# Optimization experiments

Hardware: AMD Instinct MI355X
Metric: run time of the kernel (lower is better)

The kernel has to match this reference:

```python
import jax, jax.numpy as jnp
import numpy as np

D_MODEL = 1024
NUM_HEADS = 16
D_K = D_MODEL // NUM_HEADS
B, S = 2, 2048
NEG = -1e9


def setup_inputs() -> dict:
    key = jax.random.key(0)
    ks = jax.random.split(key, 12)
    scale = 1.0 / np.sqrt(D_MODEL)
    inp = {
        'q': jax.random.normal(ks[0], (B, S, D_MODEL), jnp.float32),
        'k': jax.random.normal(ks[1], (B, S, D_MODEL), jnp.float32),
        'v': jax.random.normal(ks[2], (B, S, D_MODEL), jnp.float32),
        'mask': jax.random.randint(ks[3], (1, 1, S, S), 0, 2, jnp.int32),
        'wq_w': jax.random.normal(ks[4], (D_MODEL, D_MODEL), jnp.float32) * scale,
        'wq_b': jnp.zeros((D_MODEL,), jnp.float32),
        'wk_w': jax.random.normal(ks[5], (D_MODEL, D_MODEL), jnp.float32) * scale,
        'wk_b': jnp.zeros((D_MODEL,), jnp.float32),
        'wv_w': jax.random.normal(ks[6], (D_MODEL, D_MODEL), jnp.float32) * scale,
        'wv_b': jnp.zeros((D_MODEL,), jnp.float32),
        'wo_w': jax.random.normal(ks[7], (D_MODEL, D_MODEL), jnp.float32) * scale,
        'wo_b': jnp.zeros((D_MODEL,), jnp.float32),
    }
    return inp


def _split_heads(x):
    # [B,S,D] -> [B,H,S,d_k]
    b, s, _ = x.shape
    return x.reshape(b, s, NUM_HEADS, D_K).transpose(0, 2, 1, 3)


def reference(q, k, v, mask, wq_w, wq_b, wk_w, wk_b, wv_w, wv_b, wo_w, wo_b):
    # torch Linear: y = x @ W.T + b
    qh = _split_heads(q @ wq_w.T + wq_b)
    kh = _split_heads(k @ wk_w.T + wk_b)
    vh = _split_heads(v @ wv_w.T + wv_b)
    scores = jnp.einsum('bhqd,bhkd->bhqk', qh, kh) / jnp.sqrt(jnp.float32(D_K))
    scores = jnp.where(mask == 0, jnp.float32(NEG), scores)
    attn = jax.nn.softmax(scores, axis=-1)  # dropout p=0 (eval): no-op
    x = jnp.einsum('bhqk,bhkd->bhqd', attn, vh)
    x = x.transpose(0, 2, 1, 3).reshape(q.shape[0], q.shape[1], D_MODEL)
    return x @ wo_w.T + wo_b
```

## Files before the change

### kernel.cpp

```cpp
#include <hip/hip_runtime.h>
#include <hip/hip_bf16.h>
#include <stdint.h>

#define S_LEN  2048
#define DMODEL 1024
#define NHEADS 16
#define DKH    64
#define KDIM   1024

typedef __bf16 bf16x8 __attribute__((ext_vector_type(8)));
typedef float  floatx4 __attribute__((ext_vector_type(4)));
typedef unsigned short ushort8v __attribute__((ext_vector_type(8)));

__device__ inline void gll16(const __bf16* g, const __bf16* l) {
    __builtin_amdgcn_global_load_lds(
        (const __attribute__((address_space(1))) void*)g,
        (__attribute__((address_space(3))) void*)l, 16, 0, 0);
}

__device__ inline float fast_exp2(float x) {
#if __has_builtin(__builtin_amdgcn_exp2f)
    return __builtin_amdgcn_exp2f(x);
#else
    return exp2f(x);
#endif
}

__global__ __launch_bounds__(256) void convert_all_kernel(
    const float* __restrict__ q, const float* __restrict__ k, const float* __restrict__ v,
    const float* __restrict__ wq, const float* __restrict__ wk, const float* __restrict__ wv,
    const float* __restrict__ wo, __bf16* __restrict__ out) {
    const size_t i8 = ((size_t)blockIdx.x * 256 + threadIdx.x) * 8;
    const float* src;
    if (i8 < 4194304u)        src = q  + i8;
    else if (i8 < 8388608u)   src = k  + (i8 - 4194304u);
    else if (i8 < 12582912u)  src = v  + (i8 - 8388608u);
    else if (i8 < 13631488u)  src = wq + (i8 - 12582912u);
    else if (i8 < 14680064u)  src = wk + (i8 - 13631488u);
    else if (i8 < 15728640u)  src = wv + (i8 - 14680064u);
    else                      src = wo + (i8 - 15728640u);
    floatx4 a = *(const floatx4*)src;
    floatx4 b = *(const floatx4*)(src + 4);
    bf16x8 r;
#pragma unroll
    for (int i = 0; i < 4; ++i) { r[i] = (__bf16)a[i]; r[i + 4] = (__bf16)b[i]; }
    *(bf16x8*)(out + i8) = r;
}

__global__ __launch_bounds__(256) void maskpack_kernel(const int* __restrict__ M,
                                                       uint64_t* __restrict__ P) {
    const size_t i = (size_t)blockIdx.x * 256 + threadIdx.x;
    uint64_t bits = __ballot(M[i] != 0);
    if ((threadIdx.x & 63) == 0) P[i >> 6] = bits;
}

__global__ __launch_bounds__(256) void qkv_gemm(
    const __bf16* __restrict__ qb, const __bf16* __restrict__ kb, const __bf16* __restrict__ vb,
    const __bf16* __restrict__ wqw, const __bf16* __restrict__ wkw, const __bf16* __restrict__ wvw,
    const float* __restrict__ biasq, const float* __restrict__ biask, const float* __restrict__ biasv,
    __bf16* __restrict__ qh, __bf16* __restrict__ kh, __bf16* __restrict__ vt) {
    __shared__ __align__(16) __bf16 As[2 * 128 * 32];
    __shared__ __align__(16) __bf16 Bs[2 * 128 * 32];

    const int lane = threadIdx.x & 63;
    const int wave = threadIdx.x >> 6;
    const int quad = lane >> 4;
    const int l15  = lane & 15;

    const int bid = blockIdx.x;
    const int job = bid >> 8;
    const int tt  = bid & 255;
    const __bf16* A; const __bf16* Bm; const float* bias; __bf16* C;
    int bx, by, MODE;
    if (job == 0)      { A = qb;  Bm = wqw; bias = biasq; C = qh; bx = tt & 7;  by = tt >> 3; MODE = 0; }
    else if (job == 1) { A = kb;  Bm = wkw; bias = biask; C = kh; bx = tt & 7;  by = tt >> 3; MODE = 0; }
    else               { A = wvw; Bm = vb;  bias = biasv; C = vt; bx = tt & 31; by = tt >> 5; MODE = 1; }

    const int m_t = by * 128, n_t = bx * 128;
    const int m0w = (wave >> 1) * 64, n0w = (wave & 1) * 64;

    const int sp = wave >> 1;
    const int sr = (wave & 1) * 64;
    const int lrow = lane >> 2;
    const int scol = ((lane & 3) ^ (lrow & 3)) * 8;

    floatx4 acc[4][4];
#pragma unroll
    for (int i = 0; i < 4; ++i)
#pragma unroll
        for (int j = 0; j < 4; ++j)
            acc[i][j] = (floatx4){0.f, 0.f, 0.f, 0.f};

    for (int kk = 0; kk < KDIM; kk += 64) {
#pragma unroll
        for (int c = 0; c < 4; ++c) {
            const int row = sr + c * 16 + lrow;
            gll16(A + (size_t)(m_t + row) * KDIM + kk + sp * 32 + scol,
                  As + (sp * 128 + sr + c * 16) * 32);
            gll16(Bm + (size_t)(n_t + row) * KDIM + kk + sp * 32 + scol,
                  Bs + (sp * 128 + sr + c * 16) * 32);
        }
        __syncthreads();
        const int cq = (quad ^ (l15 & 3)) * 8;
#pragma unroll
        for (int p = 0; p < 2; ++p) {
            bf16x8 af[4], bfr[4];
#pragma unroll
            for (int i = 0; i < 4; ++i)
                af[i] = *(const bf16x8*)(As + (p * 128 + m0w + i * 16 + l15) * 32 + cq);
#pragma unroll
            for (int j = 0; j < 4; ++j)
                bfr[j] = *(const bf16x8*)(Bs + (p * 128 + n0w + j * 16 + l15) * 32 + cq);
#pragma unroll
            for (int i = 0; i < 4; ++i)
#pragma unroll
                for (int j = 0; j < 4; ++j)
                    acc[i][j] = __builtin_amdgcn_mfma_f32_16x16x32_bf16(af[i], bfr[j], acc[i][j], 0, 0, 0);
        }
        __syncthreads();
    }

#pragma unroll
    for (int j = 0; j < 4; ++j) {
        const int n = n_t + n0w + j * 16 + l15;
        float bn = (MODE == 1) ? 0.f : bias[n];
#pragma unroll
        for (int i = 0; i < 4; ++i) {
#pragma unroll
            for (int r = 0; r < 4; ++r) {
                const int m = m_t + m0w + i * 16 + quad * 4 + r;
                float bv = (MODE == 1) ? bias[m] : bn;
                float v = acc[i][j][r] + bv;
                size_t off;
                if (MODE == 0) {
                    off = ((size_t)((m >> 11) * 16 + (n >> 6)) * 2048 + (m & 2047)) * 64 + (n & 63);
                } else {
                    off = ((size_t)((n >> 11) * 16 + (m >> 6)) * 64 + (m & 63)) * 2048 + (n & 2047);
                }
                C[off] = (__bf16)v;
            }
        }
    }
}

__global__ __launch_bounds__(256) void gemm_out(const __bf16* __restrict__ A,
                                                const __bf16* __restrict__ Bm,
                                                const float* __restrict__ bias,
                                                float* __restrict__ C) {
    __shared__ __align__(16) __bf16 As[2 * 128 * 32];
    __shared__ __align__(16) __bf16 Bs[2 * 64 * 32];

    const int lane = threadIdx.x & 63;
    const int wave = threadIdx.x >> 6;
    const int quad = lane >> 4;
    const int l15  = lane & 15;
    const int m_t = blockIdx.y * 128, n_t = blockIdx.x * 64;
    const int m0w = (wave >> 1) * 64, n0w = (wave & 1) * 32;

    const int lrow = lane >> 2;
    const int scol = ((lane & 3) ^ (lrow & 3)) * 8;

    floatx4 acc[4][2];
#pragma unroll
    for (int i = 0; i < 4; ++i)
#pragma unroll
        for (int j = 0; j < 2; ++j)
            acc[i][j] = (floatx4){0.f, 0.f, 0.f, 0.f};

    for (int kk = 0; kk < KDIM; kk += 64) {
#pragma unroll
        for (int u = 0; u < 6; ++u) {
            const int pi = wave * 6 + u;
            if (pi < 16) {
                const int panel = pi >> 3, rb = pi & 7;
                gll16(A + (size_t)(m_t + rb * 16 + lrow) * KDIM + kk + panel * 32 + scol,
                      As + (panel * 128 + rb * 16) * 32);
            } else {
                const int qi = pi - 16, panel = qi >> 2, rb = qi & 3;
                gll16(Bm + (size_t)(n_t + rb * 16 + lrow) * KDIM + kk + panel * 32 + scol,
                      Bs + (panel * 64 + rb * 16) * 32);
            }
        }
        __syncthreads();
        const int cq = (quad ^ (l15 & 3)) * 8;
#pragma unroll
        for (int p = 0; p < 2; ++p) {
            bf16x8 af[4], bfr[2];
#pragma unroll
            for (int i = 0; i < 4; ++i)
                af[i] = *(const bf16x8*)(As + (p * 128 + m0w + i * 16 + l15) * 32 + cq);
#pragma unroll
            for (int j = 0; j < 2; ++j)
                bfr[j] = *(const bf16x8*)(Bs + (p * 64 + n0w + j * 16 + l15) * 32 + cq);
#pragma unroll
            for (int i = 0; i < 4; ++i)
#pragma unroll
                for (int j = 0; j < 2; ++j)
                    acc[i][j] = __builtin_amdgcn_mfma_f32_16x16x32_bf16(af[i], bfr[j], acc[i][j], 0, 0, 0);
        }
        __syncthreads();
    }

#pragma unroll
    for (int j = 0; j < 2; ++j) {
        const int n = n_t + n0w + j * 16 + l15;
        const float bn = bias[n];
#pragma unroll
        for (int i = 0; i < 4; ++i)
#pragma unroll
            for (int r = 0; r < 4; ++r) {
                const int m = m_t + m0w + i * 16 + quad * 4 + r;
                C[(size_t)m * 1024 + n] = acc[i][j][r] + bn;
            }
    }
}

__global__ __launch_bounds__(256, 4) void attn_kernel(const __bf16* __restrict__ Qh,
                                                      const __bf16* __restrict__ Kh,
                                                      const __bf16* __restrict__ Vt,
                                                      const uint64_t* __restrict__ PM,
                                                      __bf16* __restrict__ X) {
    __shared__ __align__(16) __bf16 Ks[2][4096];
    __shared__ __align__(16) __bf16 Vs[2][4096];

    const int lane = threadIdx.x & 63;
    const int wave = threadIdx.x >> 6;
    const int quad = lane >> 4;
    const int l15  = lane & 15;
    const int l7   = l15 & 7;

    const int bid  = blockIdx.x;
    const int xcd  = bid & 7;
    const int slot = bid >> 3;
    const int grp  = xcd * 4 + (slot >> 5);
    const int qt   = slot & 31;
    const int b = grp >> 4, h = grp & 15;
    const int q0 = qt * 64 + wave * 16;

    const __bf16* Qb = Qh + (size_t)(b * NHEADS + h) * S_LEN * DKH;
    const __bf16* Kb = Kh + (size_t)(b * NHEADS + h) * S_LEN * DKH;
    const __bf16* Vb = Vt + (size_t)(b * NHEADS + h) * DKH * S_LEN;
    const uint64_t* pr = PM + (size_t)(q0 + l15) * (S_LEN / 64);

    const float cs = 0.18033688011112042f;
    const float MB = 4.0f;

    size_t offK[2], offV[2];
#pragma unroll
    for (int i = 0; i < 2; ++i) {
        const int s = wave * 128 + i * 64 + lane;
        const int r = s >> 3, cp = s & 7, c = cp ^ (r & 7);
        const int kr = (r >> 5) * 32 + ((r >> 4) & 1) * 4 + ((r >> 2) & 3) * 8 + (r & 3);
        offK[i] = (size_t)kr * DKH + c * 8;
        offV[i] = (size_t)r * S_LEN + c * 8;
    }

    bf16x8 qf[2];
#pragma unroll
    for (int c = 0; c < 2; ++c)
        qf[c] = *(const bf16x8*)(Qb + (size_t)(q0 + l15) * DKH + c * 32 + quad * 8);

    bf16x8 ones;
#pragma unroll
    for (int i = 0; i < 8; ++i) ones[i] = (__bf16)1.0f;

    floatx4 o[4], osum;
#pragma unroll
    for (int f = 0; f < 4; ++f) o[f] = (floatx4){0.f, 0.f, 0.f, 0.f};
    osum = (floatx4){0.f, 0.f, 0.f, 0.f};

    auto stage = [&](int p, int key0) {
#pragma unroll
        for (int i = 0; i < 2; ++i) {
            gll16(Kb + (size_t)key0 * DKH + offK[i], &Ks[p][(wave * 128 + i * 64) * 8]);
            gll16(Vb + key0 + offV[i],               &Vs[p][(wave * 128 + i * 64) * 8]);
        }
    };

    stage(0, 0);
    uint2 mwc = *(const uint2*)(pr);
    for (int kt = 0; kt < 32; ++kt) {
        const int p = kt & 1;
        __syncthreads();
        if (kt < 31) stage(p ^ 1, (kt + 1) * 64);
        const uint2 mw = mwc;
        if (kt < 31) mwc = *(const uint2*)(pr + kt + 1);

        bf16x8 kf[4][2];
#pragma unroll
        for (int t = 0; t < 4; ++t)
#pragma unroll
            for (int hh = 0; hh < 2; ++hh) {
                const int cp = ((hh * 4 + quad) ^ l7) * 8;
                kf[t][hh] = *(const bf16x8*)&Ks[p][(t * 16 + l15) * 64 + cp];
            }

        floatx4 st[4];
#pragma unroll
        for (int t = 0; t < 4; ++t) {
            floatx4 z = (floatx4){0.f, 0.f, 0.f, 0.f};
            z = __builtin_amdgcn_mfma_f32_16x16x32_bf16(kf[t][0], qf[0], z, 0, 0, 0);
            z = __builtin_amdgcn_mfma_f32_16x16x32_bf16(kf[t][1], qf[1], z, 0, 0, 0);
            st[t] = z;
        }

        bf16x8 pw[2];
#pragma unroll
        for (int w = 0; w < 2; ++w) {
            const uint32_t byte = (w ? mw.y : mw.x) >> (quad * 8);
            bf16x8 pb;
#pragma unroll
            for (int half = 0; half < 2; ++half) {
                const int t = w * 2 + half;
#pragma unroll
                for (int r = 0; r < 4; ++r) {
                    const int idx = half * 4 + r;
                    float e = fast_exp2(fmaf(st[t][r], cs, -MB));
                    const int sgn = ((int)(byte << (31 - idx))) >> 31;
                    e = __builtin_bit_cast(float, __builtin_bit_cast(int, e) & sgn);
                    pb[half * 4 + r] = (__bf16)e;
                }
            }
            pw[w] = pb;
        }

#pragma unroll
        for (int w = 0; w < 2; ++w) {
            const int cp = ((w * 4 + quad) ^ l7) * 8;
#pragma unroll
            for (int f = 0; f < 4; ++f) {
                bf16x8 vf = *(const bf16x8*)&Vs[p][(f * 16 + l15) * 64 + cp];
                o[f] = __builtin_amdgcn_mfma_f32_16x16x32_bf16(vf, pw[w], o[f], 0, 0, 0);
            }
            osum = __builtin_amdgcn_mfma_f32_16x16x32_bf16(ones, pw[w], osum, 0, 0, 0);
        }
    }

    const float lsum = osum[0];
    const float inv = (lsum > 0.f) ? (1.f / lsum) : 0.f;

    __syncthreads();
    unsigned short* xw = (unsigned short*)&Ks[0][0] + wave * (16 * 80);
#pragma unroll
    for (int f = 0; f < 4; ++f)
#pragma unroll
        for (int r = 0; r < 4; ++r) {
            __bf16 bv = (__bf16)(o[f][r] * inv);
            xw[l15 * 80 + f * 16 + quad * 4 + r] = __builtin_bit_cast(unsigned short, bv);
        }
#pragma unroll
    for (int it = 0; it < 2; ++it) {
        const int ql = it * 8 + (lane >> 3);
        const int dseg = (lane & 7) * 8;
        ushort8v vv = *(const ushort8v*)&xw[ql * 80 + dseg];
        unsigned short* dst = (unsigned short*)X +
            (size_t)(b * S_LEN + q0 + ql) * DMODEL + h * DKH + dseg;
        *(ushort8v*)dst = vv;
    }
}

extern "C" void kernel_launch(void* const* d_in, const int* in_sizes, int n_in,
                              void* d_out, int out_size, void* d_ws, size_t ws_size,
                              hipStream_t stream) {
    const float* q   = (const float*)d_in[0];
    const float* k   = (const float*)d_in[1];
    const float* v   = (const float*)d_in[2];
    const int*   msk = (const int*)d_in[3];
    const float* wq  = (const float*)d_in[4];
    const float* wqb = (const float*)d_in[5];
    const float* wk  = (const float*)d_in[6];
    const float* wkb = (const float*)d_in[7];
    const float* wv  = (const float*)d_in[8];
    const float* wvb = (const float*)d_in[9];
    const float* wo  = (const float*)d_in[10];
    const float* wob = (const float*)d_in[11];

    char* ws = (char*)d_ws;
    __bf16*   qh   = (__bf16*)(ws);
    __bf16*   kh   = (__bf16*)(ws + 8388608);
    __bf16*   vt   = (__bf16*)(ws + 16777216);
    uint64_t* pm   = (uint64_t*)(ws + 25165824);
    __bf16*   cb   = (__bf16*)(ws + 25690112);
    __bf16*   qb   = cb;
    __bf16*   kb   = cb + 4194304;
    __bf16*   vb   = cb + 8388608;
    __bf16*   wqbf = cb + 12582912;
    __bf16*   wkbf = cb + 13631488;
    __bf16*   wvbf = cb + 14680064;
    __bf16*   wobf = cb + 15728640;
    __bf16*   xa   = qb;

    convert_all_kernel<<<8192, 256, 0, stream>>>(q, k, v, wq, wk, wv, wo, cb);
    maskpack_kernel<<<16384, 256, 0, stream>>>(msk, pm);
    qkv_gemm<<<768, 256, 0, stream>>>(qb, kb, vb, wqbf, wkbf, wvbf, wqb, wkb, wvb, qh, kh, vt);
    attn_kernel<<<1024, 256, 0, stream>>>(qh, kh, vt, pm, xa);
    gemm_out<<<dim3(16, 32), 256, 0, stream>>>(xa, wobf, wob, (float*)d_out);
}
```

Measured before the change: 274.8 us.

## Fuse prep kernels, shrink QKV GEMM tile to 128x64, use sbfe for mask bits

```diff
diff --git a/kernel.cpp b/kernel.cpp
--- a/kernel.cpp
+++ b/kernel.cpp
@@ -26,41 +26,49 @@
 #endif
 }
 
-__global__ __launch_bounds__(256) void convert_all_kernel(
+__device__ inline int bit_sign(uint32_t v, int idx) {
+#if __has_builtin(__builtin_amdgcn_sbfe)
+    return __builtin_amdgcn_sbfe((int)v, (uint32_t)idx, 1u);
+#else
+    return ((int)(v << (31 - idx))) >> 31;
+#endif
+}
+
+__global__ __launch_bounds__(256) void prep_kernel(
     const float* __restrict__ q, const float* __restrict__ k, const float* __restrict__ v,
     const float* __restrict__ wq, const float* __restrict__ wk, const float* __restrict__ wv,
-    const float* __restrict__ wo, __bf16* __restrict__ out) {
-    const size_t i8 = ((size_t)blockIdx.x * 256 + threadIdx.x) * 8;
-    const float* src;
-    if (i8 < 4194304u)        src = q  + i8;
-    else if (i8 < 8388608u)   src = k  + (i8 - 4194304u);
-    else if (i8 < 12582912u)  src = v  + (i8 - 8388608u);
-    else if (i8 < 13631488u)  src = wq + (i8 - 12582912u);
-    else if (i8 < 14680064u)  src = wk + (i8 - 13631488u);
-    else if (i8 < 15728640u)  src = wv + (i8 - 14680064u);
-    else                      src = wo + (i8 - 15728640u);
-    floatx4 a = *(const floatx4*)src;
-    floatx4 b = *(const floatx4*)(src + 4);
-    bf16x8 r;
-#pragma unroll
-    for (int i = 0; i < 4; ++i) { r[i] = (__bf16)a[i]; r[i + 4] = (__bf16)b[i]; }
-    *(bf16x8*)(out + i8) = r;
-}
-
-__global__ __launch_bounds__(256) void maskpack_kernel(const int* __restrict__ M,
-                                                       uint64_t* __restrict__ P) {
-    const size_t i = (size_t)blockIdx.x * 256 + threadIdx.x;
-    uint64_t bits = __ballot(M[i] != 0);
-    if ((threadIdx.x & 63) == 0) P[i >> 6] = bits;
-}
-
-__global__ __launch_bounds__(256) void qkv_gemm(
+    const float* __restrict__ wo, __bf16* __restrict__ out,
+    const int* __restrict__ M, uint64_t* __restrict__ P) {
+    if (blockIdx.x < 8192) {
+        const size_t i8 = ((size_t)blockIdx.x * 256 + threadIdx.x) * 8;
+        const float* src;
+        if (i8 < 4194304u)        src = q  + i8;
+        else if (i8 < 8388608u)   src = k  + (i8 - 4194304u);
+        else if (i8 < 12582912u)  src = v  + (i8 - 8388608u);
+        else if (i8 < 13631488u)  src = wq + (i8 - 12582912u);
+        else if (i8 < 14680064u)  src = wk + (i8 - 13631488u);
+        else if (i8 < 15728640u)  src = wv + (i8 - 14680064u);
+        else                      src = wo + (i8 - 15728640u);
+        floatx4 a = *(const floatx4*)src;
+        floatx4 b = *(const floatx4*)(src + 4);
+        bf16x8 r;
+#pragma unroll
+        for (int i = 0; i < 4; ++i) { r[i] = (__bf16)a[i]; r[i + 4] = (__bf16)b[i]; }
+        *(bf16x8*)(out + i8) = r;
+    } else {
+        const size_t i = ((size_t)(blockIdx.x - 8192)) * 256 + threadIdx.x;
+        uint64_t bits = __ballot(M[i] != 0);
+        if ((threadIdx.x & 63) == 0) P[i >> 6] = bits;
+    }
+}
+
+__global__ __launch_bounds__(256, 5) void qkv_gemm(
     const __bf16* __restrict__ qb, const __bf16* __restrict__ kb, const __bf16* __restrict__ vb,
     const __bf16* __restrict__ wqw, const __bf16* __restrict__ wkw, const __bf16* __restrict__ wvw,
     const float* __restrict__ biasq, const float* __restrict__ biask, const float* __restrict__ biasv,
     __bf16* __restrict__ qh, __bf16* __restrict__ kh, __bf16* __restrict__ vt) {
     __shared__ __align__(16) __bf16 As[2 * 128 * 32];
-    __shared__ __align__(16) __bf16 Bs[2 * 128 * 32];
+    __shared__ __align__(16) __bf16 Bs[2 * 64 * 32];
 
     const int lane = threadIdx.x & 63;
     const int wave = threadIdx.x >> 6;
@@ -68,60 +76,63 @@
     const int l15  = lane & 15;
 
     const int bid = blockIdx.x;
-    const int job = bid >> 8;
-    const int tt  = bid & 255;
+    const int job = bid >> 9;
+    const int tt  = bid & 511;
     const __bf16* A; const __bf16* Bm; const float* bias; __bf16* C;
     int bx, by, MODE;
-    if (job == 0)      { A = qb;  Bm = wqw; bias = biasq; C = qh; bx = tt & 7;  by = tt >> 3; MODE = 0; }
-    else if (job == 1) { A = kb;  Bm = wkw; bias = biask; C = kh; bx = tt & 7;  by = tt >> 3; MODE = 0; }
-    else               { A = wvw; Bm = vb;  bias = biasv; C = vt; bx = tt & 31; by = tt >> 5; MODE = 1; }
-
-    const int m_t = by * 128, n_t = bx * 128;
-    const int m0w = (wave >> 1) * 64, n0w = (wave & 1) * 64;
-
-    const int sp = wave >> 1;
-    const int sr = (wave & 1) * 64;
+    if (job == 0)      { A = qb;  Bm = wqw; bias = biasq; C = qh; bx = tt & 15; by = tt >> 4; MODE = 0; }
+    else if (job == 1) { A = kb;  Bm = wkw; bias = biask; C = kh; bx = tt & 15; by = tt >> 4; MODE = 0; }
+    else               { A = wvw; Bm = vb;  bias = biasv; C = vt; bx = tt & 63; by = tt >> 6; MODE = 1; }
+
+    const int m_t = by * 128, n_t = bx * 64;
+    const int m0w = (wave >> 1) * 64, n0w = (wave & 1) * 32;
+
     const int lrow = lane >> 2;
     const int scol = ((lane & 3) ^ (lrow & 3)) * 8;
 
-    floatx4 acc[4][4];
+    floatx4 acc[4][2];
 #pragma unroll
     for (int i = 0; i < 4; ++i)
 #pragma unroll
-        for (int j = 0; j < 4; ++j)
+        for (int j = 0; j < 2; ++j)
             acc[i][j] = (floatx4){0.f, 0.f, 0.f, 0.f};
 
     for (int kk = 0; kk < KDIM; kk += 64) {
 #pragma unroll
-        for (int c = 0; c < 4; ++c) {
-            const int row = sr + c * 16 + lrow;
-            gll16(A + (size_t)(m_t + row) * KDIM + kk + sp * 32 + scol,
-                  As + (sp * 128 + sr + c * 16) * 32);
-            gll16(Bm + (size_t)(n_t + row) * KDIM + kk + sp * 32 + scol,
-                  Bs + (sp * 128 + sr + c * 16) * 32);
+        for (int u = 0; u < 6; ++u) {
+            const int pi = wave * 6 + u;
+            if (pi < 16) {
+                const int panel = pi >> 3, rb = pi & 7;
+                gll16(A + (size_t)(m_t + rb * 16 + lrow) * KDIM + kk + panel * 32 + scol,
+                      As + (panel * 128 + rb * 16) * 32);
+            } else {
+                const int qi = pi - 16, panel = qi >> 2, rb = qi & 3;
+                gll16(Bm + (size_t)(n_t + rb * 16 + lrow) * KDIM + kk + panel * 32 + scol,
+                      Bs + (panel * 64 + rb * 16) * 32);
+            }
         }
         __syncthreads();
         const int cq = (quad ^ (l15 & 3)) * 8;
 #pragma unroll
         for (int p = 0; p < 2; ++p) {
-            bf16x8 af[4], bfr[4];
+            bf16x8 af[4], bfr[2];
 #pragma unroll
             for (int i = 0; i < 4; ++i)
                 af[i] = *(const bf16x8*)(As + (p * 128 + m0w + i * 16 + l15) * 32 + cq);
 #pragma unroll
-            for (int j = 0; j < 4; ++j)
-                bfr[j] = *(const bf16x8*)(Bs + (p * 128 + n0w + j * 16 + l15) * 32 + cq);
+            for (int j = 0; j < 2; ++j)
+                bfr[j] = *(const bf16x8*)(Bs + (p * 64 + n0w + j * 16 + l15) * 32 + cq);
 #pragma unroll
             for (int i = 0; i < 4; ++i)
 #pragma unroll
-                for (int j = 0; j < 4; ++j)
+                for (int j = 0; j < 2; ++j)
                     acc[i][j] = __builtin_amdgcn_mfma_f32_16x16x32_bf16(af[i], bfr[j], acc[i][j], 0, 0, 0);
         }
         __syncthreads();
     }
 
 #pragma unroll
-    for (int j = 0; j < 4; ++j) {
+    for (int j = 0; j < 2; ++j) {
         const int n = n_t + n0w + j * 16 + l15;
         float bn = (MODE == 1) ? 0.f : bias[n];
 #pragma unroll
@@ -316,7 +327,7 @@
                 for (int r = 0; r < 4; ++r) {
                     const int idx = half * 4 + r;
                     float e = fast_exp2(fmaf(st[t][r], cs, -MB));
-                    const int sgn = ((int)(byte << (31 - idx))) >> 31;
+                    const int sgn = bit_sign(byte, idx);
                     e = __builtin_bit_cast(float, __builtin_bit_cast(int, e) & sgn);
                     pb[half * 4 + r] = (__bf16)e;
                 }
@@ -390,9 +401,8 @@
     __bf16*   wobf = cb + 15728640;
     __bf16*   xa   = qb;
 
-    convert_all_kernel<<<8192, 256, 0, stream>>>(q, k, v, wq, wk, wv, wo, cb);
-    maskpack_kernel<<<16384, 256, 0, stream>>>(msk, pm);
-    qkv_gemm<<<768, 256, 0, stream>>>(qb, kb, vb, wqbf, wkbf, wvbf, wqb, wkb, wvb, qh, kh, vt);
+    prep_kernel<<<24576, 256, 0, stream>>>(q, k, v, wq, wk, wv, wo, cb, msk, pm);
+    qkv_gemm<<<1536, 256, 0, stream>>>(qb, kb, vb, wqbf, wkbf, wvbf, wqb, wkb, wvb, qh, kh, vt);
     attn_kernel<<<1024, 256, 0, stream>>>(qh, kh, vt, pm, xa);
     gemm_out<<<dim3(16, 32), 256, 0, stream>>>(xa, wobf, wob, (float*)d_out);
 }
```

After: 266.3 us. 3.1% less time.
